# Performance work log

Measured on AMD Instinct MI355X. Metric: run time of the kernel, lower is better.

## Reference

```python
import jax, jax.numpy as jnp
import numpy as np

EPS = 1e-5

def mean_variance_norm(x):
    # x: [b,c,h,w]; torch .var(dim=2) on flattened spatial is UNBIASED (n-1)
    b, c, h, w = x.shape
    n = h * w
    mean = jnp.mean(x, axis=(2, 3), keepdims=True)
    var = jnp.sum((x - mean) ** 2, axis=(2, 3), keepdims=True) / (n - 1) + EPS
    return (x - mean) / jnp.sqrt(var)

def conv1x1(x, W, b):
    # 1x1 conv == channel-mixing matmul. W: [out_c, in_c], b: [out_c]
    return jnp.einsum('oc,bchw->bohw', W, x) + b[None, :, None, None]

def setup_inputs() -> dict:
    key = jax.random.key(0)
    ks = jax.random.split(key, 10)
    C = 512
    shp = (4, C, 64, 64)
    std = 1.0 / np.sqrt(C)
    return {
        'content': jax.random.normal(ks[0], shp, jnp.float32),
        'style': jax.random.normal(ks[1], shp, jnp.float32),
        'Wf': jax.random.normal(ks[2], (C, C), jnp.float32) * std,
        'bf': jax.random.normal(ks[3], (C,), jnp.float32) * 0.01,
        'Wg': jax.random.normal(ks[4], (C, C), jnp.float32) * std,
        'bg': jax.random.normal(ks[5], (C,), jnp.float32) * 0.01,
        'Wh': jax.random.normal(ks[6], (C, C), jnp.float32) * std,
        'bh': jax.random.normal(ks[7], (C,), jnp.float32) * 0.01,
        'Wo': jax.random.normal(ks[8], (C, C), jnp.float32) * std,
        'bo': jax.random.normal(ks[9], (C,), jnp.float32) * 0.01,
    }

def reference(content, style, Wf, bf, Wg, bg, Wh, bh, Wo, bo):
    b, c, h, w = content.shape
    hw = h * w
    F = conv1x1(mean_variance_norm(content), Wf, bf).reshape(b, c, hw)  # queries
    G = conv1x1(mean_variance_norm(style), Wg, bg).reshape(b, c, hw)    # keys
    H = conv1x1(style, Wh, bh).reshape(b, c, hw)                        # values
    # S[b,n,m] = sum_c F[b,c,n] * G[b,c,m]  (unscaled attention scores)
    S = jnp.einsum('bcn,bcm->bnm', F, G)
    S = jax.nn.softmax(S, axis=-1)
    # O[b,c,n] = sum_m H[b,c,m] * S[b,n,m]
    O = jnp.einsum('bcm,bnm->bcn', H, S).reshape(b, c, h, w)
    O = conv1x1(O, Wo, bo)
    return O + content
```

## Files before the change

### kernel.cpp

```cpp
#include <hip/hip_runtime.h>

#define C 512
#define HW 4096
#define EPSV 1e-5f

typedef _Float16 fp16x8 __attribute__((ext_vector_type(8)));
typedef _Float16 fp16x4 __attribute__((ext_vector_type(4)));
typedef float f32x4 __attribute__((ext_vector_type(4)));

#define OFF_MC    (0)
#define OFF_RC    (8192)
#define OFF_MS    (16384)
#define OFF_RS    (24576)
#define OFF_BETAF (32768)
#define OFF_V     (40960)
#define OFF_BZ    (49152)
#define OFF_T     (65536)
#define OFF_SP    (131072)
#define OFF_A     (OFF_SP + 2097152)
#define OFF_WZ    (OFF_A + 1048576)
#define OFF_XCT   (OFF_WZ + 1048576)
#define OFF_XST   (OFF_XCT + 16777216)
#define OFF_KT    (OFF_XST + 16777216)
#define OFF_HM    (OFF_KT + 16777216)
#define OFF_ML    (OFF_HM + 16777216)
#define OFF_S     (OFF_ML + 8388608)

#define FT_IDX(n, c) ((((size_t)((n) >> 4) * 16 + ((c) >> 5)) * 512) + \
                      ((((c) >> 3) & 3) * 128) + (((n) & 15) * 8) + ((c) & 7))

#define SFT_IDX(n, m) ((((size_t)((n) >> 4) * 128 + ((m) >> 5)) * 512) + \
                       ((((m) >> 3) & 3) * 128) + (((n) & 15) * 8) + ((m) & 7))


__global__ void transpose_stats_kernel(const float* __restrict__ xc, const float* __restrict__ xs,
                                       char* __restrict__ ws)
{
    int bx = blockIdx.x;
    int tensor = bx >> 11, b = (bx >> 9) & 3, c0 = ((bx >> 6) & 7) * 64, n0 = (bx & 63) * 64;
    const float* src = tensor ? xs : xc;
    _Float16* dst = (_Float16*)(ws + (tensor ? OFF_XST : OFF_XCT));
    float2* part = (float2*)(ws + OFF_SP);

    __shared__ _Float16 tile[64][72];
    __shared__ float pS[64][16], pSS[64][16];

    int tid = threadIdx.x, w = tid >> 6, lane = tid & 63, cq = lane >> 4, l16 = lane & 15;
    #pragma unroll
    for (int k = 0; k < 4; k++) {
        int cr = w * 16 + k * 4 + cq;
        int nf = l16 * 4;
        float4 v = *(const float4*)(src + ((size_t)(b * C + c0 + cr)) * HW + n0 + nf);
        pS[cr][l16] = v.x + v.y + v.z + v.w;
        pSS[cr][l16] = v.x * v.x + v.y * v.y + v.z * v.z + v.w * v.w;
        tile[nf][cr] = (_Float16)v.x; tile[nf + 1][cr] = (_Float16)v.y;
        tile[nf + 2][cr] = (_Float16)v.z; tile[nf + 3][cr] = (_Float16)v.w;
    }
    __syncthreads();
    if (tid < 64) {
        float S = 0.f, SS = 0.f;
        #pragma unroll
        for (int j = 0; j < 16; j++) { S += pS[tid][j]; SS += pSS[tid][j]; }
        part[((size_t)((tensor * 4 + b) * 512 + c0 + tid)) * 64 + (n0 >> 6)] =
            make_float2(S, SS);
    }
    _Float16* dstB = dst + (size_t)b * HW * C;
    #pragma unroll
    for (int i = 0; i < 2; i++) {
        int g = tid + i * 256, row = g >> 3, c8 = (g & 7) * 8;
        int n = n0 + row, c = c0 + c8;
        *(fp16x8*)&dstB[FT_IDX(n, c)] = *(const fp16x8*)&tile[row][c8];
    }
}

__global__ void finalize_stats_kernel(char* __restrict__ ws)
{
    int ch = blockIdx.x * 256 + threadIdx.x;
    const float2* part = (const float2*)(ws + OFF_SP) + (size_t)ch * 64;
    float S = 0.f, SS = 0.f;
    for (int k = 0; k < 64; k++) { float2 v = part[k]; S += v.x; SS += v.y; }
    int tensor = ch >> 11, rem = ch & 2047;
    float m = S / (float)HW;
    float var = (SS - S * m) / (float)(HW - 1) + EPSV;
    ((float*)(ws + (tensor ? OFF_MS : OFF_MC)))[rem] = m;
    ((float*)(ws + (tensor ? OFF_RS : OFF_RC)))[rem] = rsqrtf(var);
}

__global__ void precompute_kernel(const float* __restrict__ Wf, const float* __restrict__ Wg,
                                  const float* __restrict__ Wo, const float* __restrict__ Wh,
                                  const float* __restrict__ bf, const float* __restrict__ bh,
                                  char* __restrict__ ws)
{
    float* A = (float*)(ws + OFF_A);
    _Float16* Wz16 = (_Float16*)(ws + OFF_WZ);
    float* betaf = (float*)(ws + OFF_BETAF);
    float* bz = (float*)(ws + OFF_BZ);
    const float* mc = (const float*)(ws + OFF_MC);
    const float* rc = (const float*)(ws + OFF_RC);
    int bx = blockIdx.x, t = threadIdx.x;
    if (bx < 512) {
        bool isA = bx < 256;
        int r0 = (isA ? bx : bx - 256) * 2;
        float a00 = 0.f, a01 = 0.f, a10 = 0.f, a11 = 0.f;
        for (int k = 0; k < C; k++) {
            float r0v, r1v, c0v, c1v;
            if (isA) {
                r0v = Wf[k * C + r0]; r1v = Wf[k * C + r0 + 1];
                c0v = Wg[k * C + t];  c1v = Wg[k * C + t + 256];
            } else {
                r0v = Wo[r0 * C + k]; r1v = Wo[(r0 + 1) * C + k];
                c0v = Wh[k * C + t];  c1v = Wh[k * C + t + 256];
            }
            a00 += r0v * c0v; a01 += r0v * c1v;
            a10 += r1v * c0v; a11 += r1v * c1v;
        }
        if (isA) {
            A[r0 * C + t] = a00;       A[r0 * C + t + 256] = a01;
            A[(r0 + 1) * C + t] = a10; A[(r0 + 1) * C + t + 256] = a11;
        } else {
            Wz16[FT_IDX(r0, t)] = (_Float16)a00;
            Wz16[FT_IDX(r0, t + 256)] = (_Float16)a01;
            Wz16[FT_IDX(r0 + 1, t)] = (_Float16)a10;
            Wz16[FT_IDX(r0 + 1, t + 256)] = (_Float16)a11;
        }
    } else if (bx < 520) {
        int g = (bx - 512) * 256 + t, b = g >> 9, co = g & 511;
        float acc = 0.f;
        for (int i = 0; i < C; i++) acc += Wf[co * C + i] * mc[b * C + i] * rc[b * C + i];
        betaf[g] = bf[co] - acc;
    } else {
        int co = (bx - 520) * 256 + t;
        float acc = 0.f;
        for (int i = 0; i < C; i++) acc += Wo[co * C + i] * bh[i];
        bz[co] = acc;
    }
}

__global__ void scaleA_kernel(char* __restrict__ ws)
{
    const float* __restrict__ A = (const float*)(ws + OFF_A);
    const float* __restrict__ rc = (const float*)(ws + OFF_RC);
    const float* __restrict__ rs = (const float*)(ws + OFF_RS);
    _Float16* __restrict__ As = (_Float16*)(ws + OFF_SP);

    int gid = blockIdx.x * 256 + threadIdx.x;
    int b = gid >> 15, rem = gid & 32767;
    int sub = rem >> 6, low6 = rem & 63;
    int r16 = sub >> 4, cb4 = sub & 15;
    int q = low6 >> 4, l16 = low6 & 15;
    int r = r16 * 16 + l16, j0 = (cb4 * 4 + q) * 8;

    float4 a0 = *(const float4*)&A[r * C + j0];
    float4 a1 = *(const float4*)&A[r * C + j0 + 4];
    float4 s0 = *(const float4*)&rs[b * C + j0];
    float4 s1 = *(const float4*)&rs[b * C + j0 + 4];
    float rcv = rc[b * C + r];
    fp16x8 o;
    o[0] = (_Float16)(a0.x * rcv * s0.x); o[1] = (_Float16)(a0.y * rcv * s0.y);
    o[2] = (_Float16)(a0.z * rcv * s0.z); o[3] = (_Float16)(a0.w * rcv * s0.w);
    o[4] = (_Float16)(a1.x * rcv * s1.x); o[5] = (_Float16)(a1.y * rcv * s1.y);
    o[6] = (_Float16)(a1.z * rcv * s1.z); o[7] = (_Float16)(a1.w * rcv * s1.w);
    *(fp16x8*)&As[(size_t)b * 262144 + (size_t)sub * 512 + low6 * 8] = o;
}

__global__ void precompute_v_kernel(const float* __restrict__ Wg, char* __restrict__ ws)
{
    const float* betaf = (const float*)(ws + OFF_BETAF);
    const float* rs = (const float*)(ws + OFF_RS);
    float* v = (float*)(ws + OFF_V);
    int g = blockIdx.x * 32 + (threadIdx.x >> 3);
    int b = g >> 9, j = g & 511, cq = threadIdx.x & 7;
    float acc = 0.f;
    for (int co = cq * 64; co < cq * 64 + 64; co++) acc += betaf[b * C + co] * Wg[co * C + j];
    acc += __shfl_xor(acc, 1);
    acc += __shfl_xor(acc, 2);
    acc += __shfl_xor(acc, 4);
    if (cq == 0) v[g] = rs[b * C + j] * acc;
}

__global__ void __launch_bounds__(256) prep_gemm_kernel(char* __restrict__ ws)
{
    const _Float16* __restrict__ As = (const _Float16*)(ws + OFF_SP);
    const _Float16* __restrict__ Wz16 = (const _Float16*)(ws + OFF_WZ);
    const float* __restrict__ bz = (const float*)(ws + OFF_BZ);
    const _Float16* __restrict__ xsT = (const _Float16*)(ws + OFF_XST);
    _Float16* __restrict__ Kt = (_Float16*)(ws + OFF_KT);
    _Float16* __restrict__ Hp = (_Float16*)(ws + OFF_HM);

    int bx = blockIdx.x;
    int b = bx & 3, rest = bx >> 2;
    int r128 = rest >> 5, mb = rest & 31;
    int r0 = r128 * 128, m0 = mb * 128;
    int w = threadIdx.x >> 6, lane = threadIdx.x & 63, q = lane >> 4, l16 = lane & 15;
    int wr = (w & 1) * 64, wm = (w >> 1) * 64;
    bool isK = (r0 < 512);
    int rbase = (isK ? r0 : r0 - 512) + wr;

    f32x4 zz = {0.f, 0.f, 0.f, 0.f};
    f32x4 acc[4][4];
    #pragma unroll
    for (int rt = 0; rt < 4; rt++)
        #pragma unroll
        for (int mt = 0; mt < 4; mt++) acc[rt][mt] = zz;

    const _Float16* ap = (isK ? As + (size_t)b * 262144 : Wz16)
                         + (size_t)(rbase >> 4) * 8192 + q * 128 + l16 * 8;
    const _Float16* xb = xsT + (size_t)b * HW * C
                             + (size_t)((m0 + wm) >> 4) * 8192 + q * 128 + l16 * 8;

    for (int ks = 0; ks < 16; ks++) {
        fp16x8 afr[4], bfr[4];
        #pragma unroll
        for (int rt = 0; rt < 4; rt++)
            afr[rt] = *(const fp16x8*)(ap + (size_t)rt * 8192 + ks * 512);
        #pragma unroll
        for (int mt = 0; mt < 4; mt++)
            bfr[mt] = *(const fp16x8*)(xb + (size_t)(mt * 16 + ks) * 512);
        #pragma unroll
        for (int rt = 0; rt < 4; rt++)
            #pragma unroll
            for (int mt = 0; mt < 4; mt++)
                acc[rt][mt] = __builtin_amdgcn_mfma_f32_16x16x32_f16(afr[rt], bfr[mt], acc[rt][mt], 0, 0, 0);
    }

    if (isK) {
        _Float16* KtB = Kt + (size_t)b * HW * C;
        #pragma unroll
        for (int rt = 0; rt < 4; rt++)
            #pragma unroll
            for (int mt = 0; mt < 4; mt++) {
                int m = m0 + wm + mt * 16 + l16;
                int cb = r0 + wr + rt * 16 + q * 4;
                fp16x4 h;
                h[0] = (_Float16)acc[rt][mt][0]; h[1] = (_Float16)acc[rt][mt][1];
                h[2] = (_Float16)acc[rt][mt][2]; h[3] = (_Float16)acc[rt][mt][3];
                *(fp16x4*)&KtB[FT_IDX(m, cb)] = h;
            }
    } else {
        _Float16* HpB = Hp + (size_t)b * 2097152;
        #pragma unroll
        for (int rt = 0; rt < 4; rt++) {
            float bzv[4];
            #pragma unroll
            for (int reg = 0; reg < 4; reg++) bzv[reg] = bz[rbase + rt * 16 + q * 4 + reg];
            #pragma unroll
            for (int mt = 0; mt < 4; mt++) {
                int m = m0 + wm + mt * 16 + l16;
                int mbase = (m >> 3) * 128 + (m & 7);
                #pragma unroll
                for (int reg = 0; reg < 4; reg++) {
                    int co = rbase + rt * 16 + q * 4 + reg;
                    HpB[(size_t)(co >> 4) * 65536 + mbase + (co & 15) * 8] =
                        (_Float16)(acc[rt][mt][reg] + bzv[reg]);
                }
            }
        }
    }
}

__global__ void t_kernel(char* __restrict__ ws)
{
    const float* v = (const float*)(ws + OFF_V);
    const _Float16* __restrict__ xsT = (const _Float16*)(ws + OFF_XST);
    float* tG = (float*)(ws + OFF_T);
    int bx = blockIdx.x;
    int b = bx >> 6, mb = bx & 63;
    int tid = threadIdx.x, w = tid >> 6, lane = tid & 63, q = lane >> 4, l16 = lane & 15;
    int M16 = mb * 4 + w;
    const _Float16* p = xsT + (size_t)b * HW * C + (size_t)M16 * 8192 + q * 128 + l16 * 8;
    const float* vp = v + b * C + q * 8;
    float acc = 0.f;
    #pragma unroll
    for (int st = 0; st < 16; st++) {
        fp16x8 xv = *(const fp16x8*)(p + st * 512);
        float4 v0 = *(const float4*)(vp + st * 32);
        float4 v1 = *(const float4*)(vp + st * 32 + 4);
        acc += (float)xv[0] * v0.x + (float)xv[1] * v0.y + (float)xv[2] * v0.z + (float)xv[3] * v0.w
             + (float)xv[4] * v1.x + (float)xv[5] * v1.y + (float)xv[6] * v1.z + (float)xv[7] * v1.w;
    }
    acc += __shfl_xor(acc, 16);
    acc += __shfl_xor(acc, 32);
    if (q == 0) tG[b * HW + M16 * 16 + l16] = acc;
}

__global__ void __launch_bounds__(256, 4) qk_kernel(char* __restrict__ ws)
{
    const _Float16* __restrict__ xcT = (const _Float16*)(ws + OFF_XCT);
    const _Float16* __restrict__ Kt = (const _Float16*)(ws + OFF_KT);
    const float* __restrict__ tG = (const float*)(ws + OFF_T);
    float2* __restrict__ ML = (float2*)(ws + OFF_ML);
    _Float16* __restrict__ Sg = (_Float16*)(ws + OFF_S);

    int bx = blockIdx.x;
    int b = (bx >> 1) & 3, mhi = bx & 1;
    int rest = bx >> 3, mlo = rest & 15, ntile = rest >> 4;
    int m0 = (mhi * 16 + mlo) * 128, n0 = ntile * 128;
    int tid = threadIdx.x, w = tid >> 6, lane = tid & 63, q = lane >> 4, l16 = lane & 15;
    int wn = (w & 1) * 64, wm = (w >> 1) * 64;

    __shared__ char lbuf[36864];
    _Float16* Ax0 = (_Float16*)lbuf;
    _Float16* Bx0 = (_Float16*)(lbuf + 16384);

    int st = tid >> 5, so = (tid & 31) * 16;
    const _Float16* gA = xcT + (size_t)b * HW * C + ((size_t)(n0 >> 4) + st) * 8192 + so;
    const _Float16* gB = Kt + (size_t)b * HW * C + ((size_t)(m0 >> 4) + st) * 8192 + so;

    {
        fp16x8 a0 = *(const fp16x8*)(gA);
        fp16x8 a1 = *(const fp16x8*)(gA + 8);
        fp16x8 b0 = *(const fp16x8*)(gB);
        fp16x8 b1 = *(const fp16x8*)(gB + 8);
        *(fp16x8*)&Ax0[tid * 16] = a0; *(fp16x8*)&Ax0[tid * 16 + 8] = a1;
        *(fp16x8*)&Bx0[tid * 16] = b0; *(fp16x8*)&Bx0[tid * 16 + 8] = b1;
    }
    __syncthreads();

    f32x4 zz = {0.f, 0.f, 0.f, 0.f};
    f32x4 acc[4][4];
    #pragma unroll
    for (int nt = 0; nt < 4; nt++)
        #pragma unroll
        for (int mt = 0; mt < 4; mt++) acc[nt][mt] = zz;

    int aoff = ((wn >> 4)) * 512 + q * 128 + l16 * 8;
    int boff = ((wm >> 4)) * 512 + q * 128 + l16 * 8;

    for (int ks = 0; ks < 16; ks++) {
        int buf = ks & 1;
        _Float16* Axc = Ax0 + buf * 4096;
        _Float16* Bxc = Bx0 + buf * 4096;
        fp16x8 a0n, a1n, b0n, b1n;
        if (ks < 15) {
            a0n = *(const fp16x8*)(gA + (ks + 1) * 512);
            a1n = *(const fp16x8*)(gA + (ks + 1) * 512 + 8);
            b0n = *(const fp16x8*)(gB + (ks + 1) * 512);
            b1n = *(const fp16x8*)(gB + (ks + 1) * 512 + 8);
        }

        fp16x8 afr[4], bfr[4];
        #pragma unroll
        for (int nt = 0; nt < 4; nt++)
            afr[nt] = *(const fp16x8*)&Axc[aoff + nt * 512];
        #pragma unroll
        for (int mt = 0; mt < 4; mt++)
            bfr[mt] = *(const fp16x8*)&Bxc[boff + mt * 512];
        #pragma unroll
        for (int nt = 0; nt < 4; nt++)
            #pragma unroll
            for (int mt = 0; mt < 4; mt++)
                acc[nt][mt] = __builtin_amdgcn_mfma_f32_16x16x32_f16(afr[nt], bfr[mt], acc[nt][mt], 0, 0, 0);

        if (ks < 15) {
            _Float16* Axn = Ax0 + (buf ^ 1) * 4096;
            _Float16* Bxn = Bx0 + (buf ^ 1) * 4096;
            *(fp16x8*)&Axn[tid * 16] = a0n; *(fp16x8*)&Axn[tid * 16 + 8] = a1n;
            *(fp16x8*)&Bxn[tid * 16] = b0n; *(fp16x8*)&Bxn[tid * 16 + 8] = b1n;
        }
        __syncthreads();
    }

    float tv[4];
    #pragma unroll
    for (int mt = 0; mt < 4; mt++) tv[mt] = tG[b * HW + m0 + wm + mt * 16 + l16];
    #pragma unroll
    for (int nt = 0; nt < 4; nt++)
        #pragma unroll
        for (int mt = 0; mt < 4; mt++)
            #pragma unroll
            for (int reg = 0; reg < 4; reg++) acc[nt][mt][reg] += tv[mt];

    float rm[4][4], sum[4][4];
    #pragma unroll
    for (int nt = 0; nt < 4; nt++)
        #pragma unroll
        for (int reg = 0; reg < 4; reg++)
            rm[nt][reg] = fmaxf(fmaxf(acc[nt][0][reg], acc[nt][1][reg]),
                                fmaxf(acc[nt][2][reg], acc[nt][3][reg]));
    #pragma unroll
    for (int s = 1; s < 16; s <<= 1)
        #pragma unroll
        for (int nt = 0; nt < 4; nt++)
            #pragma unroll
            for (int reg = 0; reg < 4; reg++)
                rm[nt][reg] = fmaxf(rm[nt][reg], __shfl_xor(rm[nt][reg], s));
    #pragma unroll
    for (int nt = 0; nt < 4; nt++)
        #pragma unroll
        for (int reg = 0; reg < 4; reg++) sum[nt][reg] = 0.f;
    #pragma unroll
    for (int nt = 0; nt < 4; nt++)
        #pragma unroll
        for (int mt = 0; mt < 4; mt++)
            #pragma unroll
            for (int reg = 0; reg < 4; reg++) {
                float pv = __expf(acc[nt][mt][reg] - rm[nt][reg]);
                acc[nt][mt][reg] = pv;
                sum[nt][reg] += pv;
            }
    #pragma unroll
    for (int s = 1; s < 16; s <<= 1)
        #pragma unroll
        for (int nt = 0; nt < 4; nt++)
            #pragma unroll
            for (int reg = 0; reg < 4; reg++)
                sum[nt][reg] += __shfl_xor(sum[nt][reg], s);

    int tl = (m0 + wm) >> 6;
    if (l16 == 0) {
        #pragma unroll
        for (int nt = 0; nt < 4; nt++)
            #pragma unroll
            for (int reg = 0; reg < 4; reg++)
                ML[((size_t)(b * HW + n0 + wn + nt * 16 + q * 4 + reg)) * 64 + tl] =
                    make_float2(rm[nt][reg], sum[nt][reg]);
    }

    _Float16 (*Pl)[64][72] = (_Float16(*)[64][72])lbuf;
    #pragma unroll
    for (int nt = 0; nt < 4; nt++)
        #pragma unroll
        for (int mt = 0; mt < 4; mt++)
            #pragma unroll
            for (int reg = 0; reg < 4; reg++)
                Pl[w][nt * 16 + q * 4 + reg][mt * 16 + l16] = (_Float16)acc[nt][mt][reg];
    __syncthreads();
    _Float16* SgB = Sg + (size_t)b * 16777216;
    #pragma unroll
    for (int i = 0; i < 8; i++) {
        int row = i * 8 + (lane >> 3), c8 = (lane & 7) * 8;
        int n = n0 + wn + row, m = m0 + wm + c8;
        *(fp16x8*)&SgB[SFT_IDX(n, m)] = *(const fp16x8*)&Pl[w][row][c8];
    }
}

__global__ void __launch_bounds__(256) scale_kernel(char* __restrict__ ws)
{
    const float* __restrict__ mlf0 = (const float*)(ws + OFF_ML);
    float* __restrict__ Scl = (float*)(ws + OFF_XCT);
    __shared__ float mlv[64][129];
    __shared__ float Ms[64], Li[64];

    int g0 = blockIdx.x * 64;
    int tid = threadIdx.x;
    const float* mlf = mlf0 + (size_t)g0 * 128;

    #pragma unroll
    for (int i = 0; i < 8; i++) {
        int f4 = i * 256 + tid;
        int row = f4 >> 5, c4 = (f4 & 31) * 4;
        float4 v = *(const float4*)(mlf + row * 128 + c4);
        mlv[row][c4] = v.x; mlv[row][c4 + 1] = v.y;
        mlv[row][c4 + 2] = v.z; mlv[row][c4 + 3] = v.w;
    }
    __syncthreads();
    if (tid < 64) {
        float M = -1e30f;
        #pragma unroll
        for (int k = 0; k < 64; k++) M = fmaxf(M, mlv[tid][k * 2]);
        float L = 0.f;
        #pragma unroll
        for (int k = 0; k < 64; k++) L += mlv[tid][k * 2 + 1] * __expf(mlv[tid][k * 2] - M);
        Ms[tid] = M; Li[tid] = 1.f / L;
    }
    __syncthreads();
    int b = g0 >> 12, nbase = g0 & 4095;
    float* sp = Scl + (size_t)b * 262144 + nbase;
    int row = tid & 63, tsub = tid >> 6;
    #pragma unroll
    for (int pass = 0; pass < 16; pass++) {
        int tile = pass * 4 + tsub;
        sp[(size_t)tile * 4096 + row] = __expf(mlv[row][tile * 2] - Ms[row]) * Li[row];
    }
}

__global__ void __launch_bounds__(256, 4) pv_kernel(const float* __restrict__ xc,
                                                    const float* __restrict__ bo,
                                                    float* __restrict__ out,
                                                    char* __restrict__ ws)
{
    const _Float16* __restrict__ Sft = (const _Float16*)(ws + OFF_S);
    const _Float16* __restrict__ Hp = (const _Float16*)(ws + OFF_HM);
    const float* __restrict__ Scl = (const float*)(ws + OFF_XCT);

    int bx = blockIdx.x;
    int b = bx & 3, cog = (bx >> 2) & 7, ntb = bx >> 5;
    int co0 = cog * 64;
    int tid = threadIdx.x, w = tid >> 6, lane = tid & 63, q = lane >> 4, l16 = lane & 15;
    int n0w = ntb * 128 + w * 32;

    __shared__ _Float16 Hl[2][4096];

    int ln64 = lane;
    const _Float16* hsrc = Hp + (size_t)b * 2097152
                              + (size_t)((co0 >> 4) + w) * 65536 + ln64 * 8;
    const _Float16* sb = Sft + (size_t)b * 16777216
                             + (size_t)(ntb * 8 + w * 2) * 65536 + q * 128 + l16 * 8;
    const float* sc = Scl + (size_t)b * 262144 + n0w + q * 4;

    {
        fp16x8 s0 = *(const fp16x8*)(hsrc);
        fp16x8 s1 = *(const fp16x8*)(hsrc + 512);
        *(fp16x8*)&Hl[0][w * 1024 + ln64 * 8] = s0;
        *(fp16x8*)&Hl[0][w * 1024 + 512 + ln64 * 8] = s1;
    }
    __syncthreads();

    f32x4 zz = {0.f, 0.f, 0.f, 0.f};
    f32x4 acc[2][4];
    #pragma unroll
    for (int nt = 0; nt < 2; nt++)
        #pragma unroll
        for (int ct = 0; ct < 4; ct++) acc[nt][ct] = zz;

    for (int chunk = 0; chunk < 64; chunk++) {
        int buf = chunk & 1;
        fp16x8 s0n, s1n;
        if (chunk < 63) {
            s0n = *(const fp16x8*)(hsrc + (chunk + 1) * 1024);
            s1n = *(const fp16x8*)(hsrc + (chunk + 1) * 1024 + 512);
        }

        f32x4 tmp[2][4];
        #pragma unroll
        for (int km = 0; km < 2; km++) {
            fp16x8 afr[2], bfr[4];
            #pragma unroll
            for (int nt = 0; nt < 2; nt++)
                afr[nt] = *(const fp16x8*)(sb + (size_t)nt * 65536 + (chunk * 2 + km) * 512);
            #pragma unroll
            for (int ct = 0; ct < 4; ct++)
                bfr[ct] = *(const fp16x8*)&Hl[buf][ct * 1024 + (km * 4 + q) * 128 + l16 * 8];
            #pragma unroll
            for (int nt = 0; nt < 2; nt++)
                #pragma unroll
                for (int ct = 0; ct < 4; ct++)
                    tmp[nt][ct] = __builtin_amdgcn_mfma_f32_16x16x32_f16(
                        afr[nt], bfr[ct], km == 0 ? zz : tmp[nt][ct], 0, 0, 0);
        }
        float4 sv0 = *(const float4*)(sc + chunk * 4096);
        float4 sv1 = *(const float4*)(sc + chunk * 4096 + 16);
        float sva[2][4] = {{sv0.x, sv0.y, sv0.z, sv0.w}, {sv1.x, sv1.y, sv1.z, sv1.w}};
        #pragma unroll
        for (int nt = 0; nt < 2; nt++)
            #pragma unroll
            for (int ct = 0; ct < 4; ct++)
                #pragma unroll
                for (int reg = 0; reg < 4; reg++)
                    acc[nt][ct][reg] += tmp[nt][ct][reg] * sva[nt][reg];

        if (chunk < 63) {
            *(fp16x8*)&Hl[buf ^ 1][w * 1024 + ln64 * 8] = s0n;
            *(fp16x8*)&Hl[buf ^ 1][w * 1024 + 512 + ln64 * 8] = s1n;
        }
        __syncthreads();
    }

    #pragma unroll
    for (int nt = 0; nt < 2; nt++)
        #pragma unroll
        for (int ct = 0; ct < 4; ct++) {
            int co = co0 + ct * 16 + l16;
            size_t base = ((size_t)(b * C + co)) * HW + n0w + nt * 16 + q * 4;
            float4 cv = *(const float4*)&xc[base];
            float bov = bo[co];
            float4 o;
            o.x = acc[nt][ct][0] + bov + cv.x;
            o.y = acc[nt][ct][1] + bov + cv.y;
            o.z = acc[nt][ct][2] + bov + cv.z;
            o.w = acc[nt][ct][3] + bov + cv.w;
            *(float4*)&out[base] = o;
        }
}

extern "C" void kernel_launch(void* const* d_in, const int* in_sizes, int n_in,
                              void* d_out, int out_size, void* d_ws, size_t ws_size,
                              hipStream_t stream)
{
    const float* content = (const float*)d_in[0];
    const float* style   = (const float*)d_in[1];
    const float* Wf = (const float*)d_in[2];
    const float* bf = (const float*)d_in[3];
    const float* Wg = (const float*)d_in[4];
    const float* Wh = (const float*)d_in[6];
    const float* bh = (const float*)d_in[7];
    const float* Wo = (const float*)d_in[8];
    const float* bo = (const float*)d_in[9];
    float* out = (float*)d_out;
    char* ws = (char*)d_ws;

    transpose_stats_kernel<<<4096, 256, 0, stream>>>(content, style, ws);
    finalize_stats_kernel<<<16, 256, 0, stream>>>(ws);
    precompute_kernel<<<522, 256, 0, stream>>>(Wf, Wg, Wo, Wh, bf, bh, ws);
    scaleA_kernel<<<512, 256, 0, stream>>>(ws);
    precompute_v_kernel<<<64, 256, 0, stream>>>(Wg, ws);
    prep_gemm_kernel<<<1024, 256, 0, stream>>>(ws);
    t_kernel<<<256, 256, 0, stream>>>(ws);
    qk_kernel<<<4096, 256, 0, stream>>>(ws);
    scale_kernel<<<256, 256, 0, stream>>>(ws);
    pv_kernel<<<1024, 256, 0, stream>>>(content, bo, out, ws);
}
```

Measured before the change: 459.5 us.

## Restructure small prep kernels for coalesced access and split vector precompute

The partial-stats buffer becomes chunk-major so finalize reads are coalesced. The bias/beta vector products move out of precompute_kernel into a new wave-per-output vecprep kernel that uses shuffle reductions, replacing the serial per-thread loops. scaleA stages rows of A in shared memory, and precompute_v tiles Wg through shared memory with fewer blocks. These kernels are small next to the attention GEMMs, so any effect on total time is limited, and the extra launch adds overhead.

```diff
diff --git a/kernel.cpp b/kernel.cpp
--- a/kernel.cpp
+++ b/kernel.cpp
@@ -33,6 +33,7 @@
                        ((((m) >> 3) & 3) * 128) + (((n) & 15) * 8) + ((m) & 7))
 
 
+
 __global__ void transpose_stats_kernel(const float* __restrict__ xc, const float* __restrict__ xs,
                                        char* __restrict__ ws)
 {
@@ -61,7 +62,7 @@
         float S = 0.f, SS = 0.f;
         #pragma unroll
         for (int j = 0; j < 16; j++) { S += pS[tid][j]; SS += pSS[tid][j]; }
-        part[((size_t)((tensor * 4 + b) * 512 + c0 + tid)) * 64 + (n0 >> 6)] =
+        part[((size_t)(n0 >> 6)) * 4096 + (tensor * 4 + b) * 512 + c0 + tid] =
             make_float2(S, SS);
     }
     _Float16* dstB = dst + (size_t)b * HW * C;
@@ -76,9 +77,9 @@
 __global__ void finalize_stats_kernel(char* __restrict__ ws)
 {
     int ch = blockIdx.x * 256 + threadIdx.x;
-    const float2* part = (const float2*)(ws + OFF_SP) + (size_t)ch * 64;
+    const float2* part = (const float2*)(ws + OFF_SP);
     float S = 0.f, SS = 0.f;
-    for (int k = 0; k < 64; k++) { float2 v = part[k]; S += v.x; SS += v.y; }
+    for (int k = 0; k < 64; k++) { float2 v = part[(size_t)k * 4096 + ch]; S += v.x; SS += v.y; }
     int tensor = ch >> 11, rem = ch & 2047;
     float m = S / (float)HW;
     float var = (SS - S * m) / (float)(HW - 1) + EPSV;
@@ -88,94 +89,170 @@
 
 __global__ void precompute_kernel(const float* __restrict__ Wf, const float* __restrict__ Wg,
                                   const float* __restrict__ Wo, const float* __restrict__ Wh,
-                                  const float* __restrict__ bf, const float* __restrict__ bh,
                                   char* __restrict__ ws)
 {
     float* A = (float*)(ws + OFF_A);
     _Float16* Wz16 = (_Float16*)(ws + OFF_WZ);
+    int bx = blockIdx.x, t = threadIdx.x;
+    bool isA = bx < 256;
+    int r0 = (isA ? bx : bx - 256) * 2;
+    float a00 = 0.f, a01 = 0.f, a10 = 0.f, a11 = 0.f;
+    for (int k = 0; k < C; k++) {
+        float r0v, r1v, c0v, c1v;
+        if (isA) {
+            r0v = Wf[k * C + r0]; r1v = Wf[k * C + r0 + 1];
+            c0v = Wg[k * C + t];  c1v = Wg[k * C + t + 256];
+        } else {
+            r0v = Wo[r0 * C + k]; r1v = Wo[(r0 + 1) * C + k];
+            c0v = Wh[k * C + t];  c1v = Wh[k * C + t + 256];
+        }
+        a00 += r0v * c0v; a01 += r0v * c1v;
+        a10 += r1v * c0v; a11 += r1v * c1v;
+    }
+    if (isA) {
+        A[r0 * C + t] = a00;       A[r0 * C + t + 256] = a01;
+        A[(r0 + 1) * C + t] = a10; A[(r0 + 1) * C + t + 256] = a11;
+    } else {
+        Wz16[FT_IDX(r0, t)] = (_Float16)a00;
+        Wz16[FT_IDX(r0, t + 256)] = (_Float16)a01;
+        Wz16[FT_IDX(r0 + 1, t)] = (_Float16)a10;
+        Wz16[FT_IDX(r0 + 1, t + 256)] = (_Float16)a11;
+    }
+}
+
+__global__ void __launch_bounds__(256) vecprep_kernel(const float* __restrict__ Wf,
+                                                      const float* __restrict__ bf,
+                                                      const float* __restrict__ Wo,
+                                                      const float* __restrict__ bh,
+                                                      char* __restrict__ ws)
+{
+    const float* mc = (const float*)(ws + OFF_MC);
+    const float* rc = (const float*)(ws + OFF_RC);
     float* betaf = (float*)(ws + OFF_BETAF);
     float* bz = (float*)(ws + OFF_BZ);
-    const float* mc = (const float*)(ws + OFF_MC);
-    const float* rc = (const float*)(ws + OFF_RC);
-    int bx = blockIdx.x, t = threadIdx.x;
-    if (bx < 512) {
-        bool isA = bx < 256;
-        int r0 = (isA ? bx : bx - 256) * 2;
-        float a00 = 0.f, a01 = 0.f, a10 = 0.f, a11 = 0.f;
-        for (int k = 0; k < C; k++) {
-            float r0v, r1v, c0v, c1v;
-            if (isA) {
-                r0v = Wf[k * C + r0]; r1v = Wf[k * C + r0 + 1];
-                c0v = Wg[k * C + t];  c1v = Wg[k * C + t + 256];
-            } else {
-                r0v = Wo[r0 * C + k]; r1v = Wo[(r0 + 1) * C + k];
-                c0v = Wh[k * C + t];  c1v = Wh[k * C + t + 256];
-            }
-            a00 += r0v * c0v; a01 += r0v * c1v;
-            a10 += r1v * c0v; a11 += r1v * c1v;
-        }
-        if (isA) {
-            A[r0 * C + t] = a00;       A[r0 * C + t + 256] = a01;
-            A[(r0 + 1) * C + t] = a10; A[(r0 + 1) * C + t + 256] = a11;
-        } else {
-            Wz16[FT_IDX(r0, t)] = (_Float16)a00;
-            Wz16[FT_IDX(r0, t + 256)] = (_Float16)a01;
-            Wz16[FT_IDX(r0 + 1, t)] = (_Float16)a10;
-            Wz16[FT_IDX(r0 + 1, t + 256)] = (_Float16)a11;
-        }
-    } else if (bx < 520) {
-        int g = (bx - 512) * 256 + t, b = g >> 9, co = g & 511;
-        float acc = 0.f;
-        for (int i = 0; i < C; i++) acc += Wf[co * C + i] * mc[b * C + i] * rc[b * C + i];
-        betaf[g] = bf[co] - acc;
+
+    int o = blockIdx.x * 4 + (threadIdx.x >> 6);
+    int lane = threadIdx.x & 63;
+    float acc = 0.f;
+    if (o < 2048) {
+        int b = o >> 9, co = o & 511;
+        const float* wr = Wf + (size_t)co * C + lane * 8;
+        const float* mp = mc + b * C + lane * 8;
+        const float* rp = rc + b * C + lane * 8;
+        #pragma unroll
+        for (int e = 0; e < 8; e++) acc += wr[e] * mp[e] * rp[e];
     } else {
-        int co = (bx - 520) * 256 + t;
-        float acc = 0.f;
-        for (int i = 0; i < C; i++) acc += Wo[co * C + i] * bh[i];
-        bz[co] = acc;
-    }
-}
-
-__global__ void scaleA_kernel(char* __restrict__ ws)
+        int co = o - 2048;
+        const float* wr = Wo + (size_t)co * C + lane * 8;
+        const float* bp = bh + lane * 8;
+        #pragma unroll
+        for (int e = 0; e < 8; e++) acc += wr[e] * bp[e];
+    }
+    acc += __shfl_xor(acc, 1);
+    acc += __shfl_xor(acc, 2);
+    acc += __shfl_xor(acc, 4);
+    acc += __shfl_xor(acc, 8);
+    acc += __shfl_xor(acc, 16);
+    acc += __shfl_xor(acc, 32);
+    if (lane == 0) {
+        if (o < 2048) betaf[o] = bf[o & 511] - acc;
+        else bz[o - 2048] = acc;
+    }
+}
+
+__global__ void __launch_bounds__(256) scaleA_kernel(char* __restrict__ ws)
 {
     const float* __restrict__ A = (const float*)(ws + OFF_A);
     const float* __restrict__ rc = (const float*)(ws + OFF_RC);
     const float* __restrict__ rs = (const float*)(ws + OFF_RS);
     _Float16* __restrict__ As = (_Float16*)(ws + OFF_SP);
 
-    int gid = blockIdx.x * 256 + threadIdx.x;
-    int b = gid >> 15, rem = gid & 32767;
-    int sub = rem >> 6, low6 = rem & 63;
-    int r16 = sub >> 4, cb4 = sub & 15;
-    int q = low6 >> 4, l16 = low6 & 15;
-    int r = r16 * 16 + l16, j0 = (cb4 * 4 + q) * 8;
-
-    float4 a0 = *(const float4*)&A[r * C + j0];
-    float4 a1 = *(const float4*)&A[r * C + j0 + 4];
-    float4 s0 = *(const float4*)&rs[b * C + j0];
-    float4 s1 = *(const float4*)&rs[b * C + j0 + 4];
-    float rcv = rc[b * C + r];
-    fp16x8 o;
-    o[0] = (_Float16)(a0.x * rcv * s0.x); o[1] = (_Float16)(a0.y * rcv * s0.y);
-    o[2] = (_Float16)(a0.z * rcv * s0.z); o[3] = (_Float16)(a0.w * rcv * s0.w);
-    o[4] = (_Float16)(a1.x * rcv * s1.x); o[5] = (_Float16)(a1.y * rcv * s1.y);
-    o[6] = (_Float16)(a1.z * rcv * s1.z); o[7] = (_Float16)(a1.w * rcv * s1.w);
-    *(fp16x8*)&As[(size_t)b * 262144 + (size_t)sub * 512 + low6 * 8] = o;
-}
-
-__global__ void precompute_v_kernel(const float* __restrict__ Wg, char* __restrict__ ws)
+    __shared__ float At[16][516];
+    __shared__ float rsl[512];
+    __shared__ float rcl[16];
+
+    int bx = blockIdx.x;
+    int b = bx >> 5, r16 = bx & 31;
+    int r0 = r16 * 16;
+    int t = threadIdx.x;
+
+    rsl[t] = rs[b * C + t];
+    rsl[t + 256] = rs[b * C + t + 256];
+    if (t < 16) rcl[t] = rc[b * C + r0 + t];
+    {
+        int row = t >> 4, cb = (t & 15) * 32;
+        const float* src = A + (size_t)(r0 + row) * C + cb;
+        #pragma unroll
+        for (int k = 0; k < 8; k++) {
+            float4 v = *(const float4*)(src + k * 4);
+            At[row][cb + k * 4] = v.x; At[row][cb + k * 4 + 1] = v.y;
+            At[row][cb + k * 4 + 2] = v.z; At[row][cb + k * 4 + 3] = v.w;
+        }
+    }
+    __syncthreads();
+
+    _Float16* AsB = As + (size_t)b * 262144 + (size_t)r16 * 8192;
+    #pragma unroll
+    for (int round = 0; round < 4; round++) {
+        int flat = round * 2048 + t * 8;
+        int cb4 = flat >> 9, rem = flat & 511;
+        int low6 = rem >> 3;
+        int q = low6 >> 4, l16 = low6 & 15;
+        int cbase = cb4 * 32 + q * 8;
+        float rcv = rcl[l16];
+        fp16x8 o;
+        #pragma unroll
+        for (int e = 0; e < 8; e++)
+            o[e] = (_Float16)(At[l16][cbase + e] * rcv * rsl[cbase + e]);
+        *(fp16x8*)&AsB[flat] = o;
+    }
+}
+
+__global__ void __launch_bounds__(256) precompute_v_kernel(const float* __restrict__ Wg,
+                                                           char* __restrict__ ws)
 {
     const float* betaf = (const float*)(ws + OFF_BETAF);
     const float* rs = (const float*)(ws + OFF_RS);
     float* v = (float*)(ws + OFF_V);
-    int g = blockIdx.x * 32 + (threadIdx.x >> 3);
-    int b = g >> 9, j = g & 511, cq = threadIdx.x & 7;
+
+    __shared__ float bet[512];
+    __shared__ float Wgt[64][68];
+    __shared__ float pacc[4][64];
+    __shared__ float rsl[64];
+
+    int bx = blockIdx.x;
+    int b = bx >> 3, j0 = (bx & 7) * 64;
+    int t = threadIdx.x;
+
+    bet[t] = betaf[b * C + t];
+    bet[t + 256] = betaf[b * C + t + 256];
+    if (t < 64) rsl[t] = rs[b * C + j0 + t];
+
+    int j = t & 63, g = t >> 6;
     float acc = 0.f;
-    for (int co = cq * 64; co < cq * 64 + 64; co++) acc += betaf[b * C + co] * Wg[co * C + j];
-    acc += __shfl_xor(acc, 1);
-    acc += __shfl_xor(acc, 2);
-    acc += __shfl_xor(acc, 4);
-    if (cq == 0) v[g] = rs[b * C + j] * acc;
+    for (int ch = 0; ch < 8; ch++) {
+        __syncthreads();
+        {
+            int row = t >> 2, cq = (t & 3) * 16;
+            const float* src = Wg + (size_t)(ch * 64 + row) * C + j0 + cq;
+            #pragma unroll
+            for (int k = 0; k < 4; k++) {
+                float4 w4 = *(const float4*)(src + k * 4);
+                Wgt[row][cq + k * 4] = w4.x; Wgt[row][cq + k * 4 + 1] = w4.y;
+                Wgt[row][cq + k * 4 + 2] = w4.z; Wgt[row][cq + k * 4 + 3] = w4.w;
+            }
+        }
+        __syncthreads();
+        #pragma unroll
+        for (int r2 = 0; r2 < 16; r2++) {
+            int col = g * 16 + r2;
+            acc += bet[ch * 64 + col] * Wgt[col][j];
+        }
+    }
+    pacc[g][j] = acc;
+    __syncthreads();
+    if (t < 64)
+        v[b * C + j0 + t] = rsl[t] * (pacc[0][t] + pacc[1][t] + pacc[2][t] + pacc[3][t]);
 }
 
 __global__ void __launch_bounds__(256) prep_gemm_kernel(char* __restrict__ ws)
@@ -536,7 +613,7 @@
                 #pragma unroll
                 for (int ct = 0; ct < 4; ct++)
                     tmp[nt][ct] = __builtin_amdgcn_mfma_f32_16x16x32_f16(
-                        afr[nt], bfr[ct], km == 0 ? zz : tmp[nt][ct], 0, 0, 0);
+                        afr[nt], bfr[km == 0 ? ct : ct], km == 0 ? zz : tmp[nt][ct], 0, 0, 0);
         }
         float4 sv0 = *(const float4*)(sc + chunk * 4096);
         float4 sv1 = *(const float4*)(sc + chunk * 4096 + 16);
@@ -591,9 +668,10 @@
 
     transpose_stats_kernel<<<4096, 256, 0, stream>>>(content, style, ws);
     finalize_stats_kernel<<<16, 256, 0, stream>>>(ws);
-    precompute_kernel<<<522, 256, 0, stream>>>(Wf, Wg, Wo, Wh, bf, bh, ws);
-    scaleA_kernel<<<512, 256, 0, stream>>>(ws);
-    precompute_v_kernel<<<64, 256, 0, stream>>>(Wg, ws);
+    precompute_kernel<<<512, 256, 0, stream>>>(Wf, Wg, Wo, Wh, ws);
+    vecprep_kernel<<<640, 256, 0, stream>>>(Wf, bf, Wo, bh, ws);
+    scaleA_kernel<<<128, 256, 0, stream>>>(ws);
+    precompute_v_kernel<<<32, 256, 0, stream>>>(Wg, ws);
     prep_gemm_kernel<<<1024, 256, 0, stream>>>(ws);
     t_kernel<<<256, 256, 0, stream>>>(ws);
     qk_kernel<<<4096, 256, 0, stream>>>(ws);
```

After: 474.7 us. +3.3%, slower.
